# Optimization experiments

Measured on AMD Instinct MI355X. Metric: run time of the kernel, lower is better.

Reference implementation:

```python
import jax, jax.numpy as jnp
import numpy as np

K = 20          # neighbours
NEG = 0.2       # leaky_relu slope
EPS = 1e-5      # BN eps


def _knn_gather(x, k):
    # x: (B,C,N) -> neighbour features (B,C,k,N); kNN in feature space (DGCNN style)
    feat = jnp.swapaxes(x, 1, 2)                              # (B,N,C)
    sq = jnp.sum(feat * feat, axis=-1)                        # (B,N)
    inner = jnp.einsum('bic,bjc->bij', feat, feat)
    dist = sq[:, :, None] - 2.0 * inner + sq[:, None, :]      # (B,N,N)
    idx = jax.lax.top_k(-dist, k)[1]                          # (B,N,k)
    nb = jax.vmap(lambda f, i: f[i])(feat, idx)               # (B,N,k,C)
    return jnp.transpose(nb, (0, 3, 2, 1))                    # (B,C,k,N)


def _c2(W, x):
    return jnp.einsum('oc,bckn->bokn', W, x)                  # 1x1 Conv2d, no bias


def _c1(W, x):
    return jnp.einsum('oc,bcn->bon', W, x)                    # 1x1 Conv1d, no bias


def _bn(x, g, b, axes):
    # training-mode BatchNorm (batch statistics, biased var)
    m = x.mean(axis=axes, keepdims=True)
    v = x.var(axis=axes, keepdims=True)
    sh = [1] * x.ndim
    sh[1] = -1
    return g.reshape(sh) * (x - m) * jax.lax.rsqrt(v + EPS) + b.reshape(sh)


def _repsurf(x):
    # surrogate umbrella-repsurf: pointwise 3 -> 10 surface descriptor
    p = jnp.swapaxes(x, 1, 2)                                 # (B,N,3)
    c = p - p.mean(axis=1, keepdims=True)
    r = jnp.sqrt(jnp.sum(p * p, axis=-1, keepdims=True))
    f = jnp.concatenate([p, c, p * p, r], axis=-1)            # (B,N,10)
    return jnp.swapaxes(f, 1, 2)                              # (B,10,N)


def _stage(x, Wa1, Wa2, Wfn, Wec, g, b):
    # one GANN block: kNN gather -> attention edge-conv -> cat global -> conv/BN/relu -> max over k
    nb = _knn_gather(x, K)                                    # (B,C,K,N)
    gf = jax.nn.relu(_c1(Wfn, jnp.concatenate([x, nb.max(axis=2)], axis=1)))  # FoldingNet global (B,512,N)
    xr = jnp.broadcast_to(x[:, :, None, :], nb.shape)
    diff = nb - xr
    a = jax.nn.leaky_relu(_c2(Wa1, diff) + _c2(Wa2, xr), NEG)
    alpha = jax.nn.softmax(a, axis=1)                         # softmax over channel dim (torch Softmax(dim=1))
    h = jnp.transpose(jnp.concatenate([alpha * diff, xr], axis=1), (0, 1, 3, 2))  # (B,2C,N,K)
    h = jnp.concatenate([h, jnp.broadcast_to(gf[..., None], gf.shape + (K,))], axis=1)
    h = jax.nn.relu(_bn(_c2(Wec, h), g, b, (0, 2, 3)))
    return h.max(axis=-1)                                     # (B,Cout,N)


def _forward(x, wa1_1, wa1_2, wa2_1, wa2_2, wa3_1, wa3_2, wa4_1, wa4_2,
             wfn1, wfn2, wfn3, wfn4,
             wec1, wec2, wec3, wec4, wec5, wec6, wec7, wec8,
             g1, b1, g2, b2, g3, b3, g4, b4, g5, b5, g6, b6, g7, b7):
    N = x.shape[-1]
    f = _repsurf(x)                                           # (B,10,N)
    x1 = _stage(f, wa1_1, wa1_2, wfn1, wec1, g1, b1)          # (B,64,N)
    x2 = _stage(x1, wa2_1, wa2_2, wfn2, wec2, g2, b2)         # (B,64,N)
    x3 = _stage(x2, wa3_1, wa3_2, wfn3, wec3, g3, b3)         # (B,128,N)
    x4 = _stage(x3, wa4_1, wa4_2, wfn4, wec4, g4, b4)         # (B,256,N)
    h = jax.nn.relu(_bn(_c1(wec5, jnp.concatenate([x1, x2, x3, x4], axis=1)), g5, b5, (0, 2)))
    gvec = h.max(axis=-1)                                     # global max-pool (B,1024)
    h = jnp.concatenate([x3, jnp.broadcast_to(gvec[..., None], gvec.shape + (N,))], axis=1)  # (B,1152,N)
    h = jax.nn.relu(_bn(_c1(wec6, h), g6, b6, (0, 2)))
    h = jax.nn.relu(_bn(_c1(wec7, h), g7, b7, (0, 2)))
    return jax.nn.relu(_c1(wec8, h))                          # (B,out,N)


def setup_inputs():
    key = jax.random.key(0)
    B, N, OUT = 4, 2048, 50
    ks = jax.random.split(key, 32)
    def w(k_, o, i):
        return jax.random.normal(k_, (o, i), jnp.float32) / np.float32(np.sqrt(i))
    d = {'x': jax.random.normal(ks[0], (B, 3, N), jnp.float32)}
    j = 1
    for c, nm in [(10, 'wa1'), (64, 'wa2'), (64, 'wa3'), (128, 'wa4')]:
        d[nm + '_1'] = w(ks[j], c, c); j += 1
        d[nm + '_2'] = w(ks[j], c, c); j += 1
    for nm, o, i in [('wfn1', 512, 20), ('wfn2', 512, 128), ('wfn3', 512, 128), ('wfn4', 512, 256),
                     ('wec1', 64, 532), ('wec2', 64, 640), ('wec3', 128, 640), ('wec4', 256, 768),
                     ('wec5', 1024, 512), ('wec6', 512, 1152), ('wec7', 256, 512), ('wec8', OUT, 256)]:
        d[nm] = w(ks[j], o, i); j += 1
    for i, c in enumerate([64, 64, 128, 256, 1024, 512, 256]):
        d['g%d' % (i + 1)] = jnp.ones((c,), jnp.float32)
        d['b%d' % (i + 1)] = jnp.zeros((c,), jnp.float32)
    return d


def reference(x, wa1_1, wa1_2, wa2_1, wa2_2, wa3_1, wa3_2, wa4_1, wa4_2,
              wfn1, wfn2, wfn3, wfn4,
              wec1, wec2, wec3, wec4, wec5, wec6, wec7, wec8,
              g1, b1, g2, b2, g3, b3, g4, b4, g5, b5, g6, b6, g7, b7):
    return _forward(x, wa1_1, wa1_2, wa2_1, wa2_2, wa3_1, wa3_2, wa4_1, wa4_2,
                    wfn1, wfn2, wfn3, wfn4,
                    wec1, wec2, wec3, wec4, wec5, wec6, wec7, wec8,
                    g1, b1, g2, b2, g3, b3, g4, b4, g5, b5, g6, b6, g7, b7)
```

## Files before the change

### kernel.cpp

```cpp
#include <hip/hip_runtime.h>
#include <float.h>
#include <math.h>

namespace {

constexpr int BB = 4;
constexpr int NP = 2048;
constexpr int KK = 20;
constexpr float NEGS = 0.2f;
constexpr float BEPS = 1e-5f;

__global__ void k_meanx(const float* __restrict__ x, float* __restrict__ meanx){
  int bc = blockIdx.x;
  const float* p = x + (size_t)bc*NP;
  float s=0.f;
  for(int n=threadIdx.x;n<NP;n+=256) s+=p[n];
  __shared__ float red[256];
  red[threadIdx.x]=s; __syncthreads();
  for(int st=128;st>0;st>>=1){ if(threadIdx.x<st) red[threadIdx.x]+=red[threadIdx.x+st]; __syncthreads(); }
  if(threadIdx.x==0) meanx[bc]=red[0]/(float)NP;
}

__global__ void k_repsurf(const float* __restrict__ x, const float* __restrict__ meanx, float* __restrict__ f){
  int t=blockIdx.x*256+threadIdx.x;
  if(t>=BB*NP) return;
  int b=t/NP, n=t%NP;
  float p0=x[(b*3+0)*NP+n], p1=x[(b*3+1)*NP+n], p2=x[(b*3+2)*NP+n];
  float c0=p0-meanx[b*3+0], c1=p1-meanx[b*3+1], c2=p2-meanx[b*3+2];
  float r=sqrtf(p0*p0+p1*p1+p2*p2);
  float* fb=f+(size_t)b*10*NP+n;
  fb[0]=p0; fb[NP]=p1; fb[2*NP]=p2;
  fb[3*NP]=c0; fb[4*NP]=c1; fb[5*NP]=c2;
  fb[6*NP]=p0*p0; fb[7*NP]=p1*p1; fb[8*NP]=p2*p2;
  fb[9*NP]=r;
}

__global__ void k_transpose(const float* __restrict__ in, float* __restrict__ out, int R, int S, int rs, int off){
  int t=blockIdx.x*256+threadIdx.x;
  if(t>=R*S) return;
  int s=t/R, r=t%R;
  out[(size_t)s*R+r] = in[(size_t)r*rs + off + s];
}

__global__ __launch_bounds__(256) void k_trT(const float* __restrict__ in, size_t BS,
                                             float* __restrict__ out, int C){
  __shared__ float t[32][33];
  int n0=blockIdx.x*32, c0=blockIdx.y*32, b=blockIdx.z;
  int tx=threadIdx.x%32, ty=threadIdx.x/32;
  #pragma unroll
  for(int r=0;r<32;r+=8){
    int c=c0+ty+r;
    t[ty+r][tx] = (c<C)? in[(size_t)b*BS + (size_t)c*NP + n0+tx] : 0.f;
  }
  __syncthreads();
  #pragma unroll
  for(int r=0;r<32;r+=8){
    int n=n0+ty+r, c=c0+tx;
    if(c<C) out[((size_t)b*NP + n)*C + c] = t[tx][ty+r];
  }
}

__global__ void k_sqnorm(const float* __restrict__ x, size_t BS, float* __restrict__ sq, int C){
  int t=blockIdx.x*256+threadIdx.x;
  if(t>=BB*NP)return;
  int b=t/NP, n=t%NP;
  const float* xb=x+(size_t)b*BS+n;
  float s=0.f;
  for(int c=0;c<C;c++){ float v=xb[(size_t)c*NP]; s+=v*v; }
  sq[t]=s;
}

__global__ __launch_bounds__(256) void k_dist(const float* __restrict__ xb, const float* __restrict__ sqb,
                                              float* __restrict__ D, int C){
  __shared__ __align__(16) float At[16][128];
  __shared__ __align__(16) float Bt[16][128];
  int j0 = blockIdx.x*128, i0 = blockIdx.y*128;
  int tx = threadIdx.x%16, ty = threadIdx.x/16;
  float acc[8][8]={};
  for(int c0=0;c0<C;c0+=16){
    #pragma unroll
    for(int r=0;r<8;r++){
      int tl = threadIdx.x + 256*r;
      int c = tl>>7, e = tl&127;
      int cg = c0+c;
      At[c][e] = (cg<C)? xb[(size_t)cg*NP + i0 + e] : 0.f;
    }
    #pragma unroll
    for(int r=0;r<8;r++){
      int tl = threadIdx.x + 256*r;
      int c = tl>>7, e = tl&127;
      int cg = c0+c;
      Bt[c][e] = (cg<C)? xb[(size_t)cg*NP + j0 + e] : 0.f;
    }
    __syncthreads();
    int cm = (C-c0 < 16)? (C-c0) : 16;
    for(int c=0;c<cm;c++){
      float4 a0=*(const float4*)&At[c][ty*8];
      float4 a1=*(const float4*)&At[c][ty*8+4];
      float4 b0=*(const float4*)&Bt[c][tx*8];
      float4 b1=*(const float4*)&Bt[c][tx*8+4];
      float ar[8]={a0.x,a0.y,a0.z,a0.w,a1.x,a1.y,a1.z,a1.w};
      float br[8]={b0.x,b0.y,b0.z,b0.w,b1.x,b1.y,b1.z,b1.w};
      #pragma unroll
      for(int ii=0;ii<8;ii++)
        #pragma unroll
        for(int jj=0;jj<8;jj++) acc[ii][jj] += ar[ii]*br[jj];
    }
    __syncthreads();
  }
  #pragma unroll
  for(int ii=0;ii<8;ii++){
    int i=i0+ty*8+ii;
    float si=sqb[i];
    #pragma unroll
    for(int jq=0;jq<2;jq++){
      int j=j0+tx*8+jq*4;
      float4 w;
      w.x = si + sqb[j+0] - 2.f*acc[ii][jq*4+0];
      w.y = si + sqb[j+1] - 2.f*acc[ii][jq*4+1];
      w.z = si + sqb[j+2] - 2.f*acc[ii][jq*4+2];
      w.w = si + sqb[j+3] - 2.f*acc[ii][jq*4+3];
      *(float4*)&D[(size_t)i*NP + j] = w;
    }
  }
}

__global__ __launch_bounds__(256) void k_topk(const float* __restrict__ D, int* __restrict__ out){
  int wid = threadIdx.x>>6, lane = threadIdx.x&63;
  int row = blockIdx.x*4 + wid;
  const float* d = D + (size_t)row*NP;
  unsigned long long r[20];
  #pragma unroll
  for(int q=0;q<20;q++) r[q]=~0ULL;
  for(int t=0;t<NP/64;t++){
    int j = lane + 64*t;
    float v = d[j];
    unsigned u = __float_as_uint(v);
    u = (u & 0x80000000u) ? ~u : (u | 0x80000000u);
    unsigned long long key = ((unsigned long long)u<<32) | (unsigned)j;
    #pragma unroll
    for(int q=0;q<20;q++){
      unsigned long long lo = key<r[q]?key:r[q];
      unsigned long long hi = key<r[q]?r[q]:key;
      r[q]=lo; key=hi;
    }
  }
  int* o = out + (size_t)row*KK;
  for(int kk=0;kk<KK;kk++){
    unsigned long long m = r[0];
    #pragma unroll
    for(int off=1;off<64;off<<=1){
      unsigned long long ot = __shfl_xor(m, off, 64);
      if(ot<m) m=ot;
    }
    if(lane==0) o[kk] = (int)(unsigned)(m & 0xffffffffULL);
    if(r[0]==m){
      #pragma unroll
      for(int q=0;q<19;q++) r[q]=r[q+1];
      r[19]=~0ULL;
    }
  }
}

__global__ void k_nbmax(const float* __restrict__ x, size_t BS, const int* __restrict__ idx,
                        float* __restrict__ nbm, int C){
  int t=blockIdx.x*256+threadIdx.x;
  if(t>=BB*C*NP)return;
  int n=t%NP; int bc=t/NP; int c=bc%C; int b=bc/C;
  const int* id=idx+((size_t)b*NP+n)*KK;
  const float* xr=x+(size_t)b*BS+(size_t)c*NP;
  float m=-FLT_MAX;
  for(int k=0;k<KK;k++) m=fmaxf(m,xr[id[k]]);
  nbm[t]=m;
}

template<int EPI>
__global__ __launch_bounds__(256) void k_gemm(
    const float* __restrict__ WT, int Os, int O, int Cin,
    const float* __restrict__ B1, size_t bs1, int split,
    const float* __restrict__ B2, size_t bs2,
    const float* __restrict__ ADD, size_t abs_,
    float* __restrict__ out, size_t obs, int ncols){
  __shared__ __align__(16) float At[16][64];
  __shared__ __align__(16) float Bt[16][64];
  int n0=blockIdx.x*64, o0=blockIdx.y*64, b=blockIdx.z;
  int tx=threadIdx.x%16, ty=threadIdx.x/16;
  float acc[4][4]={};
  for(int c0=0;c0<Cin;c0+=16){
    #pragma unroll
    for(int r=0;r<4;r++){
      int tl=threadIdx.x+256*r;
      int c=tl/64, e=tl%64;
      int cg=c0+c;
      At[c][e] = (cg<Cin && o0+e<O)? WT[(size_t)cg*Os + o0+e] : 0.f;
      float bv=0.f;
      if(cg<Cin){
        bv = (cg<split)? B1[(size_t)b*bs1 + (size_t)cg*ncols + n0+e]
                       : B2[(size_t)b*bs2 + (size_t)(cg-split)*ncols + n0+e];
      }
      Bt[c][e]=bv;
    }
    __syncthreads();
    int cm = (Cin-c0 < 16)? (Cin-c0) : 16;
    for(int c=0;c<cm;c++){
      float4 a4=*(const float4*)&At[c][ty*4];
      float4 b4=*(const float4*)&Bt[c][tx*4];
      float ar[4]={a4.x,a4.y,a4.z,a4.w}, br[4]={b4.x,b4.y,b4.z,b4.w};
      #pragma unroll
      for(int ii=0;ii<4;ii++)
        #pragma unroll
        for(int jj=0;jj<4;jj++) acc[ii][jj] += ar[ii]*br[jj];
    }
    __syncthreads();
  }
  #pragma unroll
  for(int ii=0;ii<4;ii++){
    int oo=o0+ty*4+ii;
    if(oo<O){
      #pragma unroll
      for(int jj=0;jj<4;jj++){
        int col=n0+tx*4+jj;
        float v=acc[ii][jj];
        if constexpr (EPI==2) v += ADD[(size_t)b*abs_ + (size_t)oo*ncols + col];
        if constexpr (EPI==4) v -= ADD[(size_t)b*abs_ + (size_t)oo*ncols + col];
        if constexpr (EPI==3) v += ADD[(size_t)b*abs_ + oo];
        if constexpr (EPI==1) v = fmaxf(v,0.f);
        out[(size_t)b*obs + (size_t)oo*ncols + col]=v;
      }
    }
  }
}

template<int C, int Cout>
__global__ __launch_bounds__(256) void k_fused(
    const float* __restrict__ xT,
    const float* __restrict__ p1T,
    const float* __restrict__ qT,
    const int* __restrict__ idx,
    const float* __restrict__ wecAT,
    const float* __restrict__ T3,
    float* __restrict__ ymx, float* __restrict__ ymn,
    float* __restrict__ sumb, float* __restrict__ ssqb){
  constexpr int CHUNK = (C+3)/4;
  __shared__ __align__(16) float W[C][64];
  __shared__ __align__(16) float Bt[C][64];
  __shared__ int sid[64*KK];
  int n0=blockIdx.x*64, o0=blockIdx.y*64, b=blockIdx.z;
  int tid=threadIdx.x, tx=tid%16, ty=tid/16;
  int col=tid>>2, sub=tid&3;
  for(int t=tid;t<C*64;t+=256){
    int c=t/64, e=t%64;
    W[c][e]=wecAT[(size_t)c*Cout + o0+e];
  }
  for(int t=tid;t<64*KK;t+=256){
    sid[t]=idx[((size_t)b*NP + n0 + t/KK)*KK + (t%KK)];
  }
  const float* t3b=T3+(size_t)b*Cout*NP;
  float t3r[4][4];
  #pragma unroll
  for(int ii=0;ii<4;ii++)
    #pragma unroll
    for(int jj=0;jj<4;jj++)
      t3r[ii][jj]=t3b[(size_t)(o0+ty*4+ii)*NP + n0+tx*4+jj];
  float mx[4][4], mn[4][4], smr[4]={0,0,0,0}, ssr[4]={0,0,0,0};
  #pragma unroll
  for(int ii=0;ii<4;ii++)
    #pragma unroll
    for(int jj=0;jj<4;jj++){ mx[ii][jj]=-FLT_MAX; mn[ii][jj]=FLT_MAX; }
  const float* xb =xT +(size_t)b*NP*C;
  const float* pb =p1T+(size_t)b*NP*C;
  const float* qb =qT +(size_t)b*NP*C;
  int n=n0+col;
  const float* qrow =qb+(size_t)n*C;
  const float* xnrow=xb+(size_t)n*C;
  const int cb=sub*CHUNK;
  __syncthreads();
  for(int k=0;k<KK;k++){
    int id=sid[col*KK+k];
    const float* prow =pb+(size_t)id*C;
    const float* xirow=xb+(size_t)id*C;
    float a[CHUNK];
    float m=-FLT_MAX;
    #pragma unroll
    for(int j=0;j<CHUNK;j++){
      int c=cb+j;
      float v = (c<C)? prow[c]+qrow[c] : -FLT_MAX;
      v = v>0.f? v : NEGS*v;
      a[j]=v; m=fmaxf(m,v);
    }
    m=fmaxf(m,__shfl_xor(m,1,64));
    m=fmaxf(m,__shfl_xor(m,2,64));
    float s=0.f;
    #pragma unroll
    for(int j=0;j<CHUNK;j++){ float e=__expf(a[j]-m); a[j]=e; s+=e; }
    s+=__shfl_xor(s,1,64);
    s+=__shfl_xor(s,2,64);
    float rs=1.f/s;
    #pragma unroll
    for(int j=0;j<CHUNK;j++){
      int c=cb+j;
      if(c<C) Bt[c][col]=a[j]*rs*(xirow[c]-xnrow[c]);
    }
    __syncthreads();
    float acc[4][4]={};
    for(int c=0;c<C;c++){
      float4 w4=*(const float4*)&W[c][ty*4];
      float4 b4=*(const float4*)&Bt[c][tx*4];
      float wr[4]={w4.x,w4.y,w4.z,w4.w}, br[4]={b4.x,b4.y,b4.z,b4.w};
      #pragma unroll
      for(int ii=0;ii<4;ii++)
        #pragma unroll
        for(int jj=0;jj<4;jj++) acc[ii][jj]+=wr[ii]*br[jj];
    }
    #pragma unroll
    for(int ii=0;ii<4;ii++){
      float rsm=0.f, rss=0.f;
      #pragma unroll
      for(int jj=0;jj<4;jj++){
        float y=acc[ii][jj]+t3r[ii][jj];
        mx[ii][jj]=fmaxf(mx[ii][jj],y);
        mn[ii][jj]=fminf(mn[ii][jj],y);
        rsm+=y; rss+=y*y;
      }
      smr[ii]+=rsm; ssr[ii]+=rss;
    }
    __syncthreads();
  }
  #pragma unroll
  for(int ii=0;ii<4;ii++){
    int oo=o0+ty*4+ii;
    float4 v4; v4.x=mx[ii][0]; v4.y=mx[ii][1]; v4.z=mx[ii][2]; v4.w=mx[ii][3];
    *(float4*)&ymx[((size_t)b*Cout+oo)*NP + n0+tx*4] = v4;
    v4.x=mn[ii][0]; v4.y=mn[ii][1]; v4.z=mn[ii][2]; v4.w=mn[ii][3];
    *(float4*)&ymn[((size_t)b*Cout+oo)*NP + n0+tx*4] = v4;
  }
  #pragma unroll
  for(int off=1;off<16;off<<=1){
    #pragma unroll
    for(int ii=0;ii<4;ii++){
      smr[ii]+=__shfl_xor(smr[ii],off,64);
      ssr[ii]+=__shfl_xor(ssr[ii],off,64);
    }
  }
  if(tx==0){
    #pragma unroll
    for(int ii=0;ii<4;ii++){
      atomicAdd(&sumb[o0+ty*4+ii], smr[ii]);
      atomicAdd(&ssqb[o0+ty*4+ii], ssr[ii]);
    }
  }
}

__global__ void k_bnprep(const float* __restrict__ sumb, const float* __restrict__ ssqb,
                         const float* __restrict__ gg, const float* __restrict__ bb,
                         float* __restrict__ sct, int Cout, float invcnt){
  int o=blockIdx.x*256+threadIdx.x;
  if(o>=Cout)return;
  float m=sumb[o]*invcnt;
  float v=ssqb[o]*invcnt-m*m;
  float s=gg[o]*rsqrtf(v+BEPS);
  sct[o]=s; sct[Cout+o]=bb[o]-s*m;
}

__global__ void k_stageout(const float* __restrict__ ymaxb, const float* __restrict__ yminb,
                           const float* __restrict__ sct, float* __restrict__ xo, int Cout, size_t obs){
  int t=blockIdx.x*256+threadIdx.x;
  if(t>=BB*Cout*NP)return;
  int n=t%NP; int r=t/NP; int o=r%Cout; int b=r/Cout;
  float s=sct[o], tt=sct[Cout+o];
  float y = s>=0.f ? fmaf(s,ymaxb[t],tt) : fmaf(s,yminb[t],tt);
  xo[(size_t)b*obs + (size_t)o*NP + n]=fmaxf(y,0.f);
}

__global__ void k_stats(const float* __restrict__ y, const float* __restrict__ gg, const float* __restrict__ bb,
                        float* __restrict__ sct, int Cch){
  int o=blockIdx.x;
  float s=0.f, ss=0.f;
  for(int t=threadIdx.x;t<BB*NP;t+=256){
    int b=t/NP, n=t%NP;
    float v=y[((size_t)b*Cch+o)*NP+n];
    s+=v; ss+=v*v;
  }
  __shared__ float r1[256], r2[256];
  r1[threadIdx.x]=s; r2[threadIdx.x]=ss;
  __syncthreads();
  for(int st=128;st>0;st>>=1){
    if(threadIdx.x<st){ r1[threadIdx.x]+=r1[threadIdx.x+st]; r2[threadIdx.x]+=r2[threadIdx.x+st]; }
    __syncthreads();
  }
  if(threadIdx.x==0){
    float m=r1[0]/(float)(BB*NP);
    float v=r2[0]/(float)(BB*NP)-m*m;
    float sc=gg[o]*rsqrtf(v+BEPS);
    sct[o]=sc; sct[Cch+o]=bb[o]-sc*m;
  }
}

__global__ void k_gvec(const float* __restrict__ y, const float* __restrict__ sct,
                       float* __restrict__ gv, int Cch, int gstride){
  int blk=blockIdx.x; int b=blk/Cch, o=blk%Cch;
  float sc=sct[o], sh=sct[Cch+o];
  float m=-FLT_MAX;
  for(int n=threadIdx.x;n<NP;n+=256) m=fmaxf(m, fmaf(sc,y[((size_t)b*Cch+o)*NP+n],sh));
  __shared__ float r[256];
  r[threadIdx.x]=m; __syncthreads();
  for(int st=128;st>0;st>>=1){ if(threadIdx.x<st) r[threadIdx.x]=fmaxf(r[threadIdx.x],r[threadIdx.x+st]); __syncthreads(); }
  if(threadIdx.x==0) gv[(size_t)b*gstride+o]=fmaxf(r[0],0.f);
}

__global__ void k_t6(const float* __restrict__ gvec, const float* __restrict__ w6, float* __restrict__ t6b){
  int t=blockIdx.x*256+threadIdx.x;
  if(t>=BB*512)return;
  int b=t/512, o=t%512;
  const float* w=w6+(size_t)o*1152+128;
  const float* gv=gvec+(size_t)b*1024;
  float s=0.f;
  for(int c=0;c<1024;c++) s+=w[c]*gv[c];
  t6b[t]=s;
}

__global__ void k_norm(float* __restrict__ y, const float* __restrict__ sct, int Cch, int total){
  int t=blockIdx.x*256+threadIdx.x;
  if(t>=total)return;
  int o=(t/NP)%Cch;
  y[t]=fmaxf(fmaf(sct[o],y[t],sct[Cch+o]),0.f);
}

}

extern "C" void kernel_launch(void* const* d_in, const int* in_sizes, int n_in,
                              void* d_out, int out_size, void* d_ws, size_t ws_size,
                              hipStream_t stream){
  const float* x   =(const float*)d_in[0];
  const float* wa_1[4]={(const float*)d_in[1],(const float*)d_in[3],(const float*)d_in[5],(const float*)d_in[7]};
  const float* wa_2[4]={(const float*)d_in[2],(const float*)d_in[4],(const float*)d_in[6],(const float*)d_in[8]};
  const float* wfn[4]={(const float*)d_in[9],(const float*)d_in[10],(const float*)d_in[11],(const float*)d_in[12]};
  const float* wec[4]={(const float*)d_in[13],(const float*)d_in[14],(const float*)d_in[15],(const float*)d_in[16]};
  const float* w5=(const float*)d_in[17];
  const float* w6=(const float*)d_in[18];
  const float* w7=(const float*)d_in[19];
  const float* w8=(const float*)d_in[20];
  const float* gs[7]; const float* bs[7];
  for(int i=0;i<7;i++){ gs[i]=(const float*)d_in[21+2*i]; bs[i]=(const float*)d_in[22+2*i]; }

  const int Cs[4]={10,64,64,128};
  const int Co[4]={64,64,128,256};
  const size_t U=(size_t)BB*NP;

  float* base=(float*)d_ws;
  size_t off=0;
  auto alloc=[&](size_t nfl)->float*{ float* p=base+off; off+=(nfl+3)&~(size_t)3; return p; };

  float* f_buf = alloc(10*U);
  float* xcat  = alloc(512*U);
  float* sq    = alloc(U);
  int*   idxb  = (int*)alloc(20*U);
  float* Qb    = alloc(128*U);
  float* P1b   = alloc(128*U);
  float* xTb   = alloc(128*U);
  float* p1Tb  = alloc(128*U);
  float* qTb   = alloc(128*U);
  float* R2    = alloc(256*U);
  float* ymx   = alloc(256*U);
  float* ymn   = alloc(256*U);
  float* sums  = alloc(2048);
  float* sct   = alloc(4096);
  float* gvecb = alloc(4096);
  float* t6b   = alloc(2048);
  float* meanxb= alloc(16);
  float* wa1T[4]; float* wa2T[4]; float* wecAT[4]; float* wecBT[4]; float* wecGT[4]; float* wfnT[4];
  for(int s=0;s<4;s++){
    int C=Cs[s], Cout=Co[s];
    wa1T[s]=alloc((size_t)C*C); wa2T[s]=alloc((size_t)C*C);
    wecAT[s]=alloc((size_t)C*Cout); wecBT[s]=alloc((size_t)C*Cout);
    wecGT[s]=alloc((size_t)512*Cout); wfnT[s]=alloc((size_t)2*C*512);
  }
  float* w5T=alloc((size_t)512*1024); float* w6mT=alloc((size_t)128*512);
  float* w7T=alloc((size_t)512*256);  float* w8T=alloc((size_t)256*50);

  float* R1 = alloc(768*U);
  float* Dbuf=R1; float* gfb=R1;
  float* y5h=R1; float* y6=R1; float* y7=R1+512*U;
  float* nbm=R2; float* T3=R2;
  (void)ws_size;

  hipMemsetAsync(sums,0,2048*sizeof(float),stream);

  for(int s=0;s<4;s++){
    int C=Cs[s], Cout=Co[s], Cin=2*C+512;
    k_transpose<<<(C*C+255)/256,256,0,stream>>>(wa_1[s],wa1T[s],C,C,C,0);
    k_transpose<<<(C*C+255)/256,256,0,stream>>>(wa_2[s],wa2T[s],C,C,C,0);
    k_transpose<<<(C*Cout+255)/256,256,0,stream>>>(wec[s],wecAT[s],Cout,C,Cin,0);
    k_transpose<<<(C*Cout+255)/256,256,0,stream>>>(wec[s],wecBT[s],Cout,C,Cin,C);
    k_transpose<<<(512*Cout+255)/256,256,0,stream>>>(wec[s],wecGT[s],Cout,512,Cin,2*C);
    k_transpose<<<(2*C*512+255)/256,256,0,stream>>>(wfn[s],wfnT[s],512,2*C,2*C,0);
  }
  k_transpose<<<(512*1024+255)/256,256,0,stream>>>(w5,w5T,1024,512,512,0);
  k_transpose<<<(128*512+255)/256,256,0,stream>>>(w6,w6mT,512,128,1152,0);
  k_transpose<<<(512*256+255)/256,256,0,stream>>>(w7,w7T,256,512,512,0);
  k_transpose<<<(256*50+255)/256,256,0,stream>>>(w8,w8T,50,256,256,0);

  k_meanx<<<12,256,0,stream>>>(x,meanxb);
  k_repsurf<<<(BB*NP+255)/256,256,0,stream>>>(x,meanxb,f_buf);

  const float* xin[4]={f_buf, xcat, xcat+(size_t)64*NP, xcat+(size_t)128*NP};
  const size_t BSs[4]={(size_t)10*NP,(size_t)512*NP,(size_t)512*NP,(size_t)512*NP};
  float* xoutb[4]={xcat, xcat+(size_t)64*NP, xcat+(size_t)128*NP, xcat+(size_t)256*NP};

  for(int s=0;s<4;s++){
    int C=Cs[s], Cout=Co[s];
    size_t BS=BSs[s];
    k_sqnorm<<<(int)((U+255)/256),256,0,stream>>>(xin[s],BS,sq,C);
    for(int b=0;b<BB;b++){
      k_dist<<<dim3(NP/128,NP/128),256,0,stream>>>(xin[s]+(size_t)b*BS, sq+(size_t)b*NP, Dbuf, C);
      k_topk<<<NP/4,256,0,stream>>>(Dbuf, idxb+(size_t)b*NP*KK);
    }
    k_nbmax<<<(int)((BB*(size_t)C*NP+255)/256),256,0,stream>>>(xin[s],BS,idxb,nbm,C);
    k_gemm<1><<<dim3(32,8,BB),256,0,stream>>>(wfnT[s],512,512,2*C, xin[s],BS,C, nbm,(size_t)C*NP,
                                              nullptr,0, gfb,(size_t)512*NP, NP);
    k_gemm<0><<<dim3(32,Cout/64,BB),256,0,stream>>>(wecGT[s],Cout,Cout,512, gfb,(size_t)512*NP,512,
                                              nullptr,0, nullptr,0, T3,(size_t)Cout*NP, NP);
    k_gemm<2><<<dim3(32,Cout/64,BB),256,0,stream>>>(wecBT[s],Cout,Cout,C, xin[s],BS,C,
                                              nullptr,0, T3,(size_t)Cout*NP, T3,(size_t)Cout*NP, NP);
    k_gemm<0><<<dim3(32,(C+63)/64,BB),256,0,stream>>>(wa1T[s],C,C,C, xin[s],BS,C,
                                              nullptr,0, nullptr,0, P1b,(size_t)C*NP, NP);
    k_gemm<4><<<dim3(32,(C+63)/64,BB),256,0,stream>>>(wa2T[s],C,C,C, xin[s],BS,C,
                                              nullptr,0, P1b,(size_t)C*NP, Qb,(size_t)C*NP, NP);
    k_trT<<<dim3(NP/32,(C+31)/32,BB),256,0,stream>>>(xin[s],BS,xTb,C);
    k_trT<<<dim3(NP/32,(C+31)/32,BB),256,0,stream>>>(P1b,(size_t)C*NP,p1Tb,C);
    k_trT<<<dim3(NP/32,(C+31)/32,BB),256,0,stream>>>(Qb,(size_t)C*NP,qTb,C);
    float* sb=sums+(size_t)s*512; float* qb=sb+256;
    if(s==0)      k_fused<10,64  ><<<dim3(NP/64,1,BB),256,0,stream>>>(xTb,p1Tb,qTb,idxb,wecAT[s],T3,ymx,ymn,sb,qb);
    else if(s==1) k_fused<64,64  ><<<dim3(NP/64,1,BB),256,0,stream>>>(xTb,p1Tb,qTb,idxb,wecAT[s],T3,ymx,ymn,sb,qb);
    else if(s==2) k_fused<64,128 ><<<dim3(NP/64,2,BB),256,0,stream>>>(xTb,p1Tb,qTb,idxb,wecAT[s],T3,ymx,ymn,sb,qb);
    else          k_fused<128,256><<<dim3(NP/64,4,BB),256,0,stream>>>(xTb,p1Tb,qTb,idxb,wecAT[s],T3,ymx,ymn,sb,qb);
    k_bnprep<<<1,256,0,stream>>>(sb,qb,gs[s],bs[s],sct,Cout,1.f/(float)((size_t)BB*NP*KK));
    k_stageout<<<(int)((BB*(size_t)Cout*NP+255)/256),256,0,stream>>>(ymx,ymn,sct,xoutb[s],Cout,(size_t)512*NP);
  }

  for(int h=0;h<2;h++){
    k_gemm<0><<<dim3(32,8,BB),256,0,stream>>>(w5T+(size_t)h*512,1024,512,512, xcat,(size_t)512*NP,512,
                                              nullptr,0, nullptr,0, y5h,(size_t)512*NP, NP);
    k_stats<<<512,256,0,stream>>>(y5h,gs[4]+h*512,bs[4]+h*512,sct,512);
    k_gvec<<<BB*512,256,0,stream>>>(y5h,sct,gvecb+h*512,512,1024);
  }
  k_t6<<<(BB*512+255)/256,256,0,stream>>>(gvecb,w6,t6b);
  k_gemm<3><<<dim3(32,8,BB),256,0,stream>>>(w6mT,512,512,128, xcat+(size_t)128*NP,(size_t)512*NP,128,
                                            nullptr,0, t6b,512, y6,(size_t)512*NP, NP);
  k_stats<<<512,256,0,stream>>>(y6,gs[5],bs[5],sct,512);
  k_norm<<<(int)((BB*(size_t)512*NP+255)/256),256,0,stream>>>(y6,sct,512,(int)(BB*512*NP));
  k_gemm<0><<<dim3(32,4,BB),256,0,stream>>>(w7T,256,256,512, y6,(size_t)512*NP,512,
                                            nullptr,0, nullptr,0, y7,(size_t)256*NP, NP);
  k_stats<<<256,256,0,stream>>>(y7,gs[6],bs[6],sct,256);
  k_norm<<<(int)((BB*(size_t)256*NP+255)/256),256,0,stream>>>(y7,sct,256,(int)(BB*256*NP));
  k_gemm<1><<<dim3(32,1,BB),256,0,stream>>>(w8T,50,50,256, y7,(size_t)256*NP,256,
                                            nullptr,0, nullptr,0, (float*)d_out,(size_t)50*NP, NP);

  (void)in_sizes; (void)n_in; (void)out_size;
}
```

Before: 2.997 ms.

## Batch kNN launches, early-exit top-k, merge GEMMs, fuse BN into consumers

Batches the distance and top-k kernels over all four batch items when workspace allows, and adds an early-exit test to the top-k insertion loop. Several 1x1 conv GEMMs are merged: the B and G halves of the edge weights, the two attention projections (written directly in transposed layout), and the two halves of conv5. A 128x128 tiled GEMM is added for the large layers. BN scale/shift and ReLU are folded into the next GEMM's input load and into a combined stage-output/transpose kernel, which removes the separate norm, transpose and bnprep passes. The full batched distance buffer needs much more workspace, and the fused paths change memory access patterns.

```diff
diff --git a/kernel.cpp b/kernel.cpp
--- a/kernel.cpp
+++ b/kernel.cpp
@@ -35,11 +35,12 @@
   fb[9*NP]=r;
 }
 
-__global__ void k_transpose(const float* __restrict__ in, float* __restrict__ out, int R, int S, int rs, int off){
+__global__ void k_transpose(const float* __restrict__ in, float* __restrict__ out,
+                            int R, int S, int rs, int off, int OS, int opos){
   int t=blockIdx.x*256+threadIdx.x;
   if(t>=R*S) return;
   int s=t/R, r=t%R;
-  out[(size_t)s*R+r] = in[(size_t)r*rs + off + s];
+  out[(size_t)s*OS + opos + r] = in[(size_t)r*rs + off + s];
 }
 
 __global__ __launch_bounds__(256) void k_trT(const float* __restrict__ in, size_t BS,
@@ -70,10 +71,15 @@
   sq[t]=s;
 }
 
-__global__ __launch_bounds__(256) void k_dist(const float* __restrict__ xb, const float* __restrict__ sqb,
-                                              float* __restrict__ D, int C){
+__global__ __launch_bounds__(256) void k_dist(const float* __restrict__ x, size_t BS,
+                                              const float* __restrict__ sq,
+                                              float* __restrict__ D, size_t Dstr, int C){
   __shared__ __align__(16) float At[16][128];
   __shared__ __align__(16) float Bt[16][128];
+  int bz=blockIdx.z;
+  const float* xb=x+(size_t)bz*BS;
+  const float* sqb=sq+(size_t)bz*NP;
+  float* Db=D+(size_t)bz*Dstr;
   int j0 = blockIdx.x*128, i0 = blockIdx.y*128;
   int tx = threadIdx.x%16, ty = threadIdx.x/16;
   float acc[8][8]={};
@@ -120,15 +126,17 @@
       w.y = si + sqb[j+1] - 2.f*acc[ii][jq*4+1];
       w.z = si + sqb[j+2] - 2.f*acc[ii][jq*4+2];
       w.w = si + sqb[j+3] - 2.f*acc[ii][jq*4+3];
-      *(float4*)&D[(size_t)i*NP + j] = w;
-    }
-  }
-}
-
-__global__ __launch_bounds__(256) void k_topk(const float* __restrict__ D, int* __restrict__ out){
+      *(float4*)&Db[(size_t)i*NP + j] = w;
+    }
+  }
+}
+
+__global__ __launch_bounds__(256) void k_topk(const float* __restrict__ D, size_t Dstr,
+                                              int* __restrict__ out){
+  int bz=blockIdx.z;
   int wid = threadIdx.x>>6, lane = threadIdx.x&63;
   int row = blockIdx.x*4 + wid;
-  const float* d = D + (size_t)row*NP;
+  const float* d = D + (size_t)bz*Dstr + (size_t)row*NP;
   unsigned long long r[20];
   #pragma unroll
   for(int q=0;q<20;q++) r[q]=~0ULL;
@@ -138,14 +146,16 @@
     unsigned u = __float_as_uint(v);
     u = (u & 0x80000000u) ? ~u : (u | 0x80000000u);
     unsigned long long key = ((unsigned long long)u<<32) | (unsigned)j;
-    #pragma unroll
-    for(int q=0;q<20;q++){
-      unsigned long long lo = key<r[q]?key:r[q];
-      unsigned long long hi = key<r[q]?r[q]:key;
-      r[q]=lo; key=hi;
-    }
-  }
-  int* o = out + (size_t)row*KK;
+    if(key < r[19]){
+      #pragma unroll
+      for(int q=0;q<20;q++){
+        unsigned long long lo = key<r[q]?key:r[q];
+        unsigned long long hi = key<r[q]?r[q]:key;
+        r[q]=lo; key=hi;
+      }
+    }
+  }
+  int* o = out + (size_t)bz*NP*KK + (size_t)row*KK;
   for(int kk=0;kk<KK;kk++){
     unsigned long long m = r[0];
     #pragma unroll
@@ -174,13 +184,15 @@
   nbm[t]=m;
 }
 
-template<int EPI>
-__global__ __launch_bounds__(256) void k_gemm(
+template<int EPI, bool INNORM>
+__global__ __launch_bounds__(256) void k_g64(
     const float* __restrict__ WT, int Os, int O, int Cin,
     const float* __restrict__ B1, size_t bs1, int split,
     const float* __restrict__ B2, size_t bs2,
-    const float* __restrict__ ADD, size_t abs_,
-    float* __restrict__ out, size_t obs, int ncols){
+    const float* __restrict__ addv, size_t avs,
+    const float* __restrict__ sct, int sctC,
+    float* __restrict__ out, size_t obs, int ncols,
+    float* __restrict__ out2, int Chalf){
   __shared__ __align__(16) float At[16][64];
   __shared__ __align__(16) float Bt[16][64];
   int n0=blockIdx.x*64, o0=blockIdx.y*64, b=blockIdx.z;
@@ -197,6 +209,7 @@
       if(cg<Cin){
         bv = (cg<split)? B1[(size_t)b*bs1 + (size_t)cg*ncols + n0+e]
                        : B2[(size_t)b*bs2 + (size_t)(cg-split)*ncols + n0+e];
+        if(INNORM) bv = fmaxf(fmaf(sct[cg],bv,sct[sctC+cg]),0.f);
       }
       Bt[c][e]=bv;
     }
@@ -217,14 +230,88 @@
   for(int ii=0;ii<4;ii++){
     int oo=o0+ty*4+ii;
     if(oo<O){
-      #pragma unroll
-      for(int jj=0;jj<4;jj++){
-        int col=n0+tx*4+jj;
-        float v=acc[ii][jj];
-        if constexpr (EPI==2) v += ADD[(size_t)b*abs_ + (size_t)oo*ncols + col];
-        if constexpr (EPI==4) v -= ADD[(size_t)b*abs_ + (size_t)oo*ncols + col];
-        if constexpr (EPI==3) v += ADD[(size_t)b*abs_ + oo];
-        if constexpr (EPI==1) v = fmaxf(v,0.f);
+      if constexpr (EPI==5){
+        #pragma unroll
+        for(int jj=0;jj<4;jj++){
+          int col=n0+tx*4+jj;
+          float v=acc[ii][jj];
+          if(oo<Chalf) out [((size_t)b*ncols+col)*Chalf + oo]       = v;
+          else         out2[((size_t)b*ncols+col)*Chalf + oo-Chalf] = v;
+        }
+      } else {
+        float bia = (EPI==3)? addv[(size_t)b*avs + oo] : 0.f;
+        #pragma unroll
+        for(int jj=0;jj<4;jj++){
+          int col=n0+tx*4+jj;
+          float v=acc[ii][jj]+bia;
+          if(EPI==1) v=fmaxf(v,0.f);
+          out[(size_t)b*obs + (size_t)oo*ncols + col]=v;
+        }
+      }
+    }
+  }
+}
+
+template<int EPI, bool INNORM>
+__global__ __launch_bounds__(256) void k_g128(
+    const float* __restrict__ WT, int Os, int O, int Cin,
+    const float* __restrict__ B1, size_t bs1, int split,
+    const float* __restrict__ B2, size_t bs2,
+    const float* __restrict__ addv, size_t avs,
+    const float* __restrict__ sct, int sctC,
+    float* __restrict__ out, size_t obs, int ncols){
+  __shared__ __align__(16) float At[16][128];
+  __shared__ __align__(16) float Bt[16][128];
+  int n0=blockIdx.x*128, o0=blockIdx.y*128, b=blockIdx.z;
+  int tx=threadIdx.x%16, ty=threadIdx.x/16;
+  float acc[8][8]={};
+  for(int c0=0;c0<Cin;c0+=16){
+    #pragma unroll
+    for(int r=0;r<8;r++){
+      int tl=threadIdx.x+256*r;
+      int c=tl>>7, e=tl&127;
+      int cg=c0+c;
+      At[c][e] = (cg<Cin && o0+e<O)? WT[(size_t)cg*Os + o0+e] : 0.f;
+    }
+    #pragma unroll
+    for(int r=0;r<8;r++){
+      int tl=threadIdx.x+256*r;
+      int c=tl>>7, e=tl&127;
+      int cg=c0+c;
+      float bv=0.f;
+      if(cg<Cin){
+        bv = (cg<split)? B1[(size_t)b*bs1 + (size_t)cg*ncols + n0+e]
+                       : B2[(size_t)b*bs2 + (size_t)(cg-split)*ncols + n0+e];
+        if(INNORM) bv = fmaxf(fmaf(sct[cg],bv,sct[sctC+cg]),0.f);
+      }
+      Bt[c][e]=bv;
+    }
+    __syncthreads();
+    int cm = (Cin-c0 < 16)? (Cin-c0) : 16;
+    for(int c=0;c<cm;c++){
+      float4 a0=*(const float4*)&At[c][ty*8];
+      float4 a1=*(const float4*)&At[c][ty*8+4];
+      float4 b0=*(const float4*)&Bt[c][tx*8];
+      float4 b1=*(const float4*)&Bt[c][tx*8+4];
+      float ar[8]={a0.x,a0.y,a0.z,a0.w,a1.x,a1.y,a1.z,a1.w};
+      float br[8]={b0.x,b0.y,b0.z,b0.w,b1.x,b1.y,b1.z,b1.w};
+      #pragma unroll
+      for(int ii=0;ii<8;ii++)
+        #pragma unroll
+        for(int jj=0;jj<8;jj++) acc[ii][jj] += ar[ii]*br[jj];
+    }
+    __syncthreads();
+  }
+  #pragma unroll
+  for(int ii=0;ii<8;ii++){
+    int oo=o0+ty*8+ii;
+    if(oo<O){
+      float bia = (EPI==3)? addv[(size_t)b*avs + oo] : 0.f;
+      #pragma unroll
+      for(int jj=0;jj<8;jj++){
+        int col=n0+tx*8+jj;
+        float v=acc[ii][jj]+bia;
+        if(EPI==1) v=fmaxf(v,0.f);
         out[(size_t)b*obs + (size_t)oo*ncols + col]=v;
       }
     }
@@ -233,17 +320,13 @@
 
 template<int C, int Cout>
 __global__ __launch_bounds__(256) void k_fused(
-    const float* __restrict__ xT,
-    const float* __restrict__ p1T,
-    const float* __restrict__ qT,
-    const int* __restrict__ idx,
-    const float* __restrict__ wecAT,
-    const float* __restrict__ T3,
+    const float* __restrict__ xT, const float* __restrict__ p1T, const float* __restrict__ a2T,
+    const int* __restrict__ idx, const float* __restrict__ wecAT, const float* __restrict__ T3,
     float* __restrict__ ymx, float* __restrict__ ymn,
     float* __restrict__ sumb, float* __restrict__ ssqb){
-  constexpr int CHUNK = (C+3)/4;
+  constexpr int CHUNK=(C+3)/4;
   __shared__ __align__(16) float W[C][64];
-  __shared__ __align__(16) float Bt[C][64];
+  __shared__ __align__(16) float Bt[C][68];
   __shared__ int sid[64*KK];
   int n0=blockIdx.x*64, o0=blockIdx.y*64, b=blockIdx.z;
   int tid=threadIdx.x, tx=tid%16, ty=tid/16;
@@ -252,9 +335,8 @@
     int c=t/64, e=t%64;
     W[c][e]=wecAT[(size_t)c*Cout + o0+e];
   }
-  for(int t=tid;t<64*KK;t+=256){
+  for(int t=tid;t<64*KK;t+=256)
     sid[t]=idx[((size_t)b*NP + n0 + t/KK)*KK + (t%KK)];
-  }
   const float* t3b=T3+(size_t)b*Cout*NP;
   float t3r[4][4];
   #pragma unroll
@@ -262,29 +344,33 @@
     #pragma unroll
     for(int jj=0;jj<4;jj++)
       t3r[ii][jj]=t3b[(size_t)(o0+ty*4+ii)*NP + n0+tx*4+jj];
+  int n=n0+col;
+  const float* xnrow=xT +((size_t)b*NP+n)*C;
+  const float* p1n  =p1T+((size_t)b*NP+n)*C;
+  const float* a2n  =a2T+((size_t)b*NP+n)*C;
+  float qv[CHUNK], xnv[CHUNK];
+  #pragma unroll
+  for(int j=0;j<CHUNK;j++){
+    int c=sub+4*j;
+    qv[j]  = (c<C)? a2n[c]-p1n[c] : 0.f;
+    xnv[j] = (c<C)? xnrow[c] : 0.f;
+  }
   float mx[4][4], mn[4][4], smr[4]={0,0,0,0}, ssr[4]={0,0,0,0};
   #pragma unroll
   for(int ii=0;ii<4;ii++)
     #pragma unroll
     for(int jj=0;jj<4;jj++){ mx[ii][jj]=-FLT_MAX; mn[ii][jj]=FLT_MAX; }
-  const float* xb =xT +(size_t)b*NP*C;
-  const float* pb =p1T+(size_t)b*NP*C;
-  const float* qb =qT +(size_t)b*NP*C;
-  int n=n0+col;
-  const float* qrow =qb+(size_t)n*C;
-  const float* xnrow=xb+(size_t)n*C;
-  const int cb=sub*CHUNK;
   __syncthreads();
   for(int k=0;k<KK;k++){
     int id=sid[col*KK+k];
-    const float* prow =pb+(size_t)id*C;
-    const float* xirow=xb+(size_t)id*C;
+    const float* prow =p1T+((size_t)b*NP+id)*C;
+    const float* xirow=xT +((size_t)b*NP+id)*C;
     float a[CHUNK];
     float m=-FLT_MAX;
     #pragma unroll
     for(int j=0;j<CHUNK;j++){
-      int c=cb+j;
-      float v = (c<C)? prow[c]+qrow[c] : -FLT_MAX;
+      int c=sub+4*j;
+      float v = (c<C)? prow[c]+qv[j] : -FLT_MAX;
       v = v>0.f? v : NEGS*v;
       a[j]=v; m=fmaxf(m,v);
     }
@@ -298,8 +384,8 @@
     float rs=1.f/s;
     #pragma unroll
     for(int j=0;j<CHUNK;j++){
-      int c=cb+j;
-      if(c<C) Bt[c][col]=a[j]*rs*(xirow[c]-xnrow[c]);
+      int c=sub+4*j;
+      if(c<C) Bt[c][col]=a[j]*rs*(xirow[c]-xnv[j]);
     }
     __syncthreads();
     float acc[4][4]={};
@@ -351,25 +437,35 @@
   }
 }
 
-__global__ void k_bnprep(const float* __restrict__ sumb, const float* __restrict__ ssqb,
-                         const float* __restrict__ gg, const float* __restrict__ bb,
-                         float* __restrict__ sct, int Cout, float invcnt){
-  int o=blockIdx.x*256+threadIdx.x;
-  if(o>=Cout)return;
-  float m=sumb[o]*invcnt;
-  float v=ssqb[o]*invcnt-m*m;
-  float s=gg[o]*rsqrtf(v+BEPS);
-  sct[o]=s; sct[Cout+o]=bb[o]-s*m;
-}
-
-__global__ void k_stageout(const float* __restrict__ ymaxb, const float* __restrict__ yminb,
-                           const float* __restrict__ sct, float* __restrict__ xo, int Cout, size_t obs){
-  int t=blockIdx.x*256+threadIdx.x;
-  if(t>=BB*Cout*NP)return;
-  int n=t%NP; int r=t/NP; int o=r%Cout; int b=r/Cout;
-  float s=sct[o], tt=sct[Cout+o];
-  float y = s>=0.f ? fmaf(s,ymaxb[t],tt) : fmaf(s,yminb[t],tt);
-  xo[(size_t)b*obs + (size_t)o*NP + n]=fmaxf(y,0.f);
+__global__ __launch_bounds__(256) void k_stageoutT(
+    const float* __restrict__ ymx, const float* __restrict__ ymn,
+    const float* __restrict__ sumb, const float* __restrict__ ssqb,
+    const float* __restrict__ gg, const float* __restrict__ bb, float invcnt,
+    float* __restrict__ xo, size_t obs, float* __restrict__ xT, int Cout, int writeT){
+  __shared__ float t[32][33];
+  int n0=blockIdx.x*32, o0=blockIdx.y*32, b=blockIdx.z;
+  int tx=threadIdx.x%32, ty=threadIdx.x/32;
+  #pragma unroll
+  for(int r=0;r<32;r+=8){
+    int o=o0+ty+r;
+    float m=sumb[o]*invcnt;
+    float v=ssqb[o]*invcnt-m*m;
+    float sc=gg[o]*rsqrtf(v+BEPS);
+    float sh=bb[o]-sc*m;
+    size_t base=((size_t)b*Cout+o)*NP + n0+tx;
+    float y = sc>=0.f ? fmaf(sc,ymx[base],sh) : fmaf(sc,ymn[base],sh);
+    y=fmaxf(y,0.f);
+    xo[(size_t)b*obs + (size_t)o*NP + n0+tx] = y;
+    t[ty+r][tx]=y;
+  }
+  if(writeT){
+    __syncthreads();
+    #pragma unroll
+    for(int r=0;r<32;r+=8){
+      int n=n0+ty+r;
+      xT[((size_t)b*NP+n)*Cout + o0+tx] = t[tx][ty+r];
+    }
+  }
 }
 
 __global__ void k_stats(const float* __restrict__ y, const float* __restrict__ gg, const float* __restrict__ bb,
@@ -417,13 +513,6 @@
   float s=0.f;
   for(int c=0;c<1024;c++) s+=w[c]*gv[c];
   t6b[t]=s;
-}
-
-__global__ void k_norm(float* __restrict__ y, const float* __restrict__ sct, int Cch, int total){
-  int t=blockIdx.x*256+threadIdx.x;
-  if(t>=total)return;
-  int o=(t/NP)%Cch;
-  y[t]=fmaxf(fmaf(sct[o],y[t],sct[Cch+o]),0.f);
 }
 
 }
@@ -446,6 +535,7 @@
   const int Cs[4]={10,64,64,128};
   const int Co[4]={64,64,128,256};
   const size_t U=(size_t)BB*NP;
+  const size_t NPNP=(size_t)NP*NP;
 
   float* base=(float*)d_ws;
   size_t off=0;
@@ -455,11 +545,9 @@
   float* xcat  = alloc(512*U);
   float* sq    = alloc(U);
   int*   idxb  = (int*)alloc(20*U);
-  float* Qb    = alloc(128*U);
-  float* P1b   = alloc(128*U);
   float* xTb   = alloc(128*U);
   float* p1Tb  = alloc(128*U);
-  float* qTb   = alloc(128*U);
+  float* a2Tb  = alloc(128*U);
   float* R2    = alloc(256*U);
   float* ymx   = alloc(256*U);
   float* ymn   = alloc(256*U);
@@ -468,37 +556,46 @@
   float* gvecb = alloc(4096);
   float* t6b   = alloc(2048);
   float* meanxb= alloc(16);
-  float* wa1T[4]; float* wa2T[4]; float* wecAT[4]; float* wecBT[4]; float* wecGT[4]; float* wfnT[4];
+  float* wa12T[4]; float* wecAT[4]; float* wecBGT[4]; float* wfnT[4];
   for(int s=0;s<4;s++){
     int C=Cs[s], Cout=Co[s];
-    wa1T[s]=alloc((size_t)C*C); wa2T[s]=alloc((size_t)C*C);
-    wecAT[s]=alloc((size_t)C*Cout); wecBT[s]=alloc((size_t)C*Cout);
-    wecGT[s]=alloc((size_t)512*Cout); wfnT[s]=alloc((size_t)2*C*512);
+    wa12T[s]=alloc((size_t)C*2*C);
+    wecAT[s]=alloc((size_t)C*Cout);
+    wecBGT[s]=alloc((size_t)(C+512)*Cout);
+    wfnT[s]=alloc((size_t)2*C*512);
   }
   float* w5T=alloc((size_t)512*1024); float* w6mT=alloc((size_t)128*512);
   float* w7T=alloc((size_t)512*256);  float* w8T=alloc((size_t)256*50);
 
-  float* R1 = alloc(768*U);
-  float* Dbuf=R1; float* gfb=R1;
-  float* y5h=R1; float* y6=R1; float* y7=R1+512*U;
+  float* R1 = alloc(1024*U);
+  float* Dbuf=R1;
+  float* gfb=R1+512*U;
+  float* y5=R1; float* y6=R1; float* y7=R1+512*U;
   float* nbm=R2; float* T3=R2;
-  (void)ws_size;
+
+  int DZ=1; float* Dall=Dbuf;
+  {
+    size_t totalF = ws_size/sizeof(float);
+    if(totalF > off && (totalF-off) >= (size_t)2048*U + 1024){
+      Dall = alloc(2048*U); DZ=4;
+    }
+  }
 
   hipMemsetAsync(sums,0,2048*sizeof(float),stream);
 
   for(int s=0;s<4;s++){
     int C=Cs[s], Cout=Co[s], Cin=2*C+512;
-    k_transpose<<<(C*C+255)/256,256,0,stream>>>(wa_1[s],wa1T[s],C,C,C,0);
-    k_transpose<<<(C*C+255)/256,256,0,stream>>>(wa_2[s],wa2T[s],C,C,C,0);
-    k_transpose<<<(C*Cout+255)/256,256,0,stream>>>(wec[s],wecAT[s],Cout,C,Cin,0);
-    k_transpose<<<(C*Cout+255)/256,256,0,stream>>>(wec[s],wecBT[s],Cout,C,Cin,C);
-    k_transpose<<<(512*Cout+255)/256,256,0,stream>>>(wec[s],wecGT[s],Cout,512,Cin,2*C);
-    k_transpose<<<(2*C*512+255)/256,256,0,stream>>>(wfn[s],wfnT[s],512,2*C,2*C,0);
-  }
-  k_transpose<<<(512*1024+255)/256,256,0,stream>>>(w5,w5T,1024,512,512,0);
-  k_transpose<<<(128*512+255)/256,256,0,stream>>>(w6,w6mT,512,128,1152,0);
-  k_transpose<<<(512*256+255)/256,256,0,stream>>>(w7,w7T,256,512,512,0);
-  k_transpose<<<(256*50+255)/256,256,0,stream>>>(w8,w8T,50,256,256,0);
+    k_transpose<<<(C*C+255)/256,256,0,stream>>>(wa_1[s],wa12T[s],C,C,C,0,2*C,0);
+    k_transpose<<<(C*C+255)/256,256,0,stream>>>(wa_2[s],wa12T[s],C,C,C,0,2*C,C);
+    k_transpose<<<(C*Cout+255)/256,256,0,stream>>>(wec[s],wecAT[s],Cout,C,Cin,0,Cout,0);
+    k_transpose<<<(C*Cout+255)/256,256,0,stream>>>(wec[s],wecBGT[s],Cout,C,Cin,C,Cout,0);
+    k_transpose<<<(512*Cout+255)/256,256,0,stream>>>(wec[s],wecBGT[s]+(size_t)C*Cout,Cout,512,Cin,2*C,Cout,0);
+    k_transpose<<<(2*C*512+255)/256,256,0,stream>>>(wfn[s],wfnT[s],512,2*C,2*C,0,512,0);
+  }
+  k_transpose<<<(512*1024+255)/256,256,0,stream>>>(w5,w5T,1024,512,512,0,1024,0);
+  k_transpose<<<(128*512+255)/256,256,0,stream>>>(w6,w6mT,512,128,1152,0,512,0);
+  k_transpose<<<(512*256+255)/256,256,0,stream>>>(w7,w7T,256,512,512,0,256,0);
+  k_transpose<<<(256*50+255)/256,256,0,stream>>>(w8,w8T,50,256,256,0,50,0);
 
   k_meanx<<<12,256,0,stream>>>(x,meanxb);
   k_repsurf<<<(BB*NP+255)/256,256,0,stream>>>(x,meanxb,f_buf);
@@ -511,50 +608,45 @@
     int C=Cs[s], Cout=Co[s];
     size_t BS=BSs[s];
     k_sqnorm<<<(int)((U+255)/256),256,0,stream>>>(xin[s],BS,sq,C);
-    for(int b=0;b<BB;b++){
-      k_dist<<<dim3(NP/128,NP/128),256,0,stream>>>(xin[s]+(size_t)b*BS, sq+(size_t)b*NP, Dbuf, C);
-      k_topk<<<NP/4,256,0,stream>>>(Dbuf, idxb+(size_t)b*NP*KK);
+    if(DZ==4){
+      k_dist<<<dim3(NP/128,NP/128,4),256,0,stream>>>(xin[s],BS,sq,Dall,NPNP,C);
+      k_topk<<<dim3(NP/4,1,4),256,0,stream>>>(Dall,NPNP,idxb);
+    } else {
+      for(int b=0;b<BB;b++){
+        k_dist<<<dim3(NP/128,NP/128,1),256,0,stream>>>(xin[s]+(size_t)b*BS,BS,sq+(size_t)b*NP,Dbuf,NPNP,C);
+        k_topk<<<dim3(NP/4,1,1),256,0,stream>>>(Dbuf,NPNP,idxb+(size_t)b*NP*KK);
+      }
     }
     k_nbmax<<<(int)((BB*(size_t)C*NP+255)/256),256,0,stream>>>(xin[s],BS,idxb,nbm,C);
-    k_gemm<1><<<dim3(32,8,BB),256,0,stream>>>(wfnT[s],512,512,2*C, xin[s],BS,C, nbm,(size_t)C*NP,
-                                              nullptr,0, gfb,(size_t)512*NP, NP);
-    k_gemm<0><<<dim3(32,Cout/64,BB),256,0,stream>>>(wecGT[s],Cout,Cout,512, gfb,(size_t)512*NP,512,
-                                              nullptr,0, nullptr,0, T3,(size_t)Cout*NP, NP);
-    k_gemm<2><<<dim3(32,Cout/64,BB),256,0,stream>>>(wecBT[s],Cout,Cout,C, xin[s],BS,C,
-                                              nullptr,0, T3,(size_t)Cout*NP, T3,(size_t)Cout*NP, NP);
-    k_gemm<0><<<dim3(32,(C+63)/64,BB),256,0,stream>>>(wa1T[s],C,C,C, xin[s],BS,C,
-                                              nullptr,0, nullptr,0, P1b,(size_t)C*NP, NP);
-    k_gemm<4><<<dim3(32,(C+63)/64,BB),256,0,stream>>>(wa2T[s],C,C,C, xin[s],BS,C,
-                                              nullptr,0, P1b,(size_t)C*NP, Qb,(size_t)C*NP, NP);
-    k_trT<<<dim3(NP/32,(C+31)/32,BB),256,0,stream>>>(xin[s],BS,xTb,C);
-    k_trT<<<dim3(NP/32,(C+31)/32,BB),256,0,stream>>>(P1b,(size_t)C*NP,p1Tb,C);
-    k_trT<<<dim3(NP/32,(C+31)/32,BB),256,0,stream>>>(Qb,(size_t)C*NP,qTb,C);
+    k_g128<1,false><<<dim3(16,4,BB),256,0,stream>>>(wfnT[s],512,512,2*C, xin[s],BS,C, nbm,(size_t)C*NP,
+                                                    nullptr,0, nullptr,0, gfb,(size_t)512*NP, NP);
+    k_g64<0,false><<<dim3(32,Cout/64,BB),256,0,stream>>>(wecBGT[s],Cout,Cout,C+512, xin[s],BS,C, gfb,(size_t)512*NP,
+                                                    nullptr,0, nullptr,0, T3,(size_t)Cout*NP, NP, nullptr,0);
+    k_g64<5,false><<<dim3(32,(2*C+63)/64,BB),256,0,stream>>>(wa12T[s],2*C,2*C,C, xin[s],BS,C, nullptr,0,
+                                                    nullptr,0, nullptr,0, p1Tb,0, NP, a2Tb,C);
+    if(s==0) k_trT<<<dim3(NP/32,1,BB),256,0,stream>>>(f_buf,BSs[0],xTb,10);
     float* sb=sums+(size_t)s*512; float* qb=sb+256;
-    if(s==0)      k_fused<10,64  ><<<dim3(NP/64,1,BB),256,0,stream>>>(xTb,p1Tb,qTb,idxb,wecAT[s],T3,ymx,ymn,sb,qb);
-    else if(s==1) k_fused<64,64  ><<<dim3(NP/64,1,BB),256,0,stream>>>(xTb,p1Tb,qTb,idxb,wecAT[s],T3,ymx,ymn,sb,qb);
-    else if(s==2) k_fused<64,128 ><<<dim3(NP/64,2,BB),256,0,stream>>>(xTb,p1Tb,qTb,idxb,wecAT[s],T3,ymx,ymn,sb,qb);
-    else          k_fused<128,256><<<dim3(NP/64,4,BB),256,0,stream>>>(xTb,p1Tb,qTb,idxb,wecAT[s],T3,ymx,ymn,sb,qb);
-    k_bnprep<<<1,256,0,stream>>>(sb,qb,gs[s],bs[s],sct,Cout,1.f/(float)((size_t)BB*NP*KK));
-    k_stageout<<<(int)((BB*(size_t)Cout*NP+255)/256),256,0,stream>>>(ymx,ymn,sct,xoutb[s],Cout,(size_t)512*NP);
-  }
-
-  for(int h=0;h<2;h++){
-    k_gemm<0><<<dim3(32,8,BB),256,0,stream>>>(w5T+(size_t)h*512,1024,512,512, xcat,(size_t)512*NP,512,
-                                              nullptr,0, nullptr,0, y5h,(size_t)512*NP, NP);
-    k_stats<<<512,256,0,stream>>>(y5h,gs[4]+h*512,bs[4]+h*512,sct,512);
-    k_gvec<<<BB*512,256,0,stream>>>(y5h,sct,gvecb+h*512,512,1024);
-  }
+    if(s==0)      k_fused<10,64  ><<<dim3(NP/64,1,BB),256,0,stream>>>(xTb,p1Tb,a2Tb,idxb,wecAT[s],T3,ymx,ymn,sb,qb);
+    else if(s==1) k_fused<64,64  ><<<dim3(NP/64,1,BB),256,0,stream>>>(xTb,p1Tb,a2Tb,idxb,wecAT[s],T3,ymx,ymn,sb,qb);
+    else if(s==2) k_fused<64,128 ><<<dim3(NP/64,2,BB),256,0,stream>>>(xTb,p1Tb,a2Tb,idxb,wecAT[s],T3,ymx,ymn,sb,qb);
+    else          k_fused<128,256><<<dim3(NP/64,4,BB),256,0,stream>>>(xTb,p1Tb,a2Tb,idxb,wecAT[s],T3,ymx,ymn,sb,qb);
+    k_stageoutT<<<dim3(NP/32,Cout/32,BB),256,0,stream>>>(ymx,ymn,sb,qb,gs[s],bs[s],
+                      1.f/(float)((size_t)BB*NP*KK), xoutb[s],(size_t)512*NP, xTb,Cout, s<3?1:0);
+  }
+
+  k_g128<0,false><<<dim3(16,8,BB),256,0,stream>>>(w5T,1024,1024,512, xcat,(size_t)512*NP,512, nullptr,0,
+                                                  nullptr,0, nullptr,0, y5,(size_t)1024*NP, NP);
+  k_stats<<<1024,256,0,stream>>>(y5,gs[4],bs[4],sct,1024);
+  k_gvec<<<BB*1024,256,0,stream>>>(y5,sct,gvecb,1024,1024);
   k_t6<<<(BB*512+255)/256,256,0,stream>>>(gvecb,w6,t6b);
-  k_gemm<3><<<dim3(32,8,BB),256,0,stream>>>(w6mT,512,512,128, xcat+(size_t)128*NP,(size_t)512*NP,128,
-                                            nullptr,0, t6b,512, y6,(size_t)512*NP, NP);
+  k_g128<3,false><<<dim3(16,4,BB),256,0,stream>>>(w6mT,512,512,128, xcat+(size_t)128*NP,(size_t)512*NP,128,
+                                                  nullptr,0, t6b,512, nullptr,0, y6,(size_t)512*NP, NP);
   k_stats<<<512,256,0,stream>>>(y6,gs[5],bs[5],sct,512);
-  k_norm<<<(int)((BB*(size_t)512*NP+255)/256),256,0,stream>>>(y6,sct,512,(int)(BB*512*NP));
-  k_gemm<0><<<dim3(32,4,BB),256,0,stream>>>(w7T,256,256,512, y6,(size_t)512*NP,512,
-                                            nullptr,0, nullptr,0, y7,(size_t)256*NP, NP);
+  k_g64<0,true><<<dim3(32,4,BB),256,0,stream>>>(w7T,256,256,512, y6,(size_t)512*NP,512, nullptr,0,
+                                                nullptr,0, sct,512, y7,(size_t)256*NP, NP, nullptr,0);
   k_stats<<<256,256,0,stream>>>(y7,gs[6],bs[6],sct,256);
-  k_norm<<<(int)((BB*(size_t)256*NP+255)/256),256,0,stream>>>(y7,sct,256,(int)(BB*256*NP));
-  k_gemm<1><<<dim3(32,1,BB),256,0,stream>>>(w8T,50,50,256, y7,(size_t)256*NP,256,
-                                            nullptr,0, nullptr,0, (float*)d_out,(size_t)50*NP, NP);
+  k_g64<1,true><<<dim3(32,1,BB),256,0,stream>>>(w8T,50,50,256, y7,(size_t)256*NP,256, nullptr,0,
+                                                nullptr,0, sct,256, (float*)d_out,(size_t)50*NP, NP, nullptr,0);
 
   (void)in_sizes; (void)n_in; (void)out_size;
 }
```

Result: faster. 2.624 ms (-12.4%).
